# Kernel optimization log

Hardware: AMD Instinct MI355X
Metric: run time of the kernel (lower is better)

Reference implementation:

```python
import jax, jax.numpy as jnp
import numpy as np

B, S, H = 16, 4096, 1024

def setup_inputs() -> dict:
    key = jax.random.key(0)
    k = jax.random.split(key, 6)
    return {
        "query": jax.random.normal(k[0], (B, 1, H), dtype=jnp.float32),
        "proj_key": jax.random.normal(k[1], (B, S, H), dtype=jnp.float32),
        "value": jax.random.normal(k[2], (B, S, 2 * H), dtype=jnp.float32),
        "Wq": jax.random.normal(k[3], (H, H), dtype=jnp.float32) * (1.0 / np.sqrt(H)),
        "we": jax.random.normal(k[4], (H,), dtype=jnp.float32) * (1.0 / np.sqrt(H)),
        "mask": jax.random.randint(k[5], (B, S), 0, 2, dtype=jnp.int32),
    }

def reference(query, proj_key, value, Wq, we, mask):
    # query: [B,1,H]; torch Linear(no bias): y = x @ W^T
    q = jnp.einsum('bqh,oh->bqo', query, Wq)            # [B,1,H]
    e = jnp.tanh(q + proj_key)                          # [B,S,H] (broadcast over S)
    scores = jnp.einsum('bsh,h->bs', e, we)             # energy_layer -> [B,S]
    scores = jnp.where(mask == 0, -jnp.inf, scores)
    alphas = jax.nn.softmax(scores, axis=-1)            # [B,S]
    context = jnp.einsum('bs,bsd->bd', alphas, value)   # bmm([B,1,S],[B,S,2H])
    return context[:, None, :], alphas[:, None, :]
```

## Files before the change

### kernel.cpp

```cpp
#include <hip/hip_runtime.h>
#include <math.h>

#define BATCH 16
#define SEQ   4096
#define HDIM  1024
#define DV    2048
#define NCH   32
#define SCH   (SEQ / NCH)
#define KFT   512

typedef float vf4 __attribute__((ext_vector_type(4)));

__device__ __forceinline__ float tanh_fast(float x) {
    float e = __expf(2.0f * x);
    return 1.0f - 2.0f * __builtin_amdgcn_rcpf(1.0f + e);
}

__device__ __forceinline__ float4 ntload4(const float4* p) {
    vf4 v = __builtin_nontemporal_load((const vf4*)p);
    return make_float4(v.x, v.y, v.z, v.w);
}

__global__ __launch_bounds__(256) void k1_q(const float* __restrict__ query,
                                            const float* __restrict__ Wq,
                                            float* __restrict__ qout) {
    int wave = threadIdx.x >> 6;
    int lane = threadIdx.x & 63;
    int o = blockIdx.x * 4 + wave;
    const float4* wq4 = (const float4*)(Wq + (size_t)o * HDIM);
    float4 w[4];
#pragma unroll
    for (int k = 0; k < 4; ++k) w[k] = wq4[k * 64 + lane];
#pragma unroll
    for (int b = 0; b < BATCH; ++b) {
        const float4* q4 = (const float4*)(query + b * HDIM);
        float acc = 0.f;
#pragma unroll
        for (int k = 0; k < 4; ++k) {
            float4 q = q4[k * 64 + lane];
            acc += w[k].x * q.x + w[k].y * q.y + w[k].z * q.z + w[k].w * q.w;
        }
#pragma unroll
        for (int off = 32; off; off >>= 1) acc += __shfl_down(acc, off, 64);
        if (lane == 0) qout[b * HDIM + o] = acc;
    }
}

__global__ __launch_bounds__(KFT) void kf_fused(const float* __restrict__ pk,
                                                const float* __restrict__ qv,
                                                const float* __restrict__ we,
                                                const int* __restrict__ mask,
                                                const float* __restrict__ value,
                                                float* __restrict__ scores,
                                                float* __restrict__ partial,
                                                float* __restrict__ chunkm,
                                                float* __restrict__ chunkz) {
    int bid = blockIdx.x;
    int b = bid >> 5;
    int c = bid & (NCH - 1);
    int s0 = c * SCH;
    int t = threadIdx.x;
    int wave = t >> 6;
    int lane = t & 63;

    __shared__ float s_sc[SCH];
    __shared__ float s_a[SCH];
    __shared__ int   s_list[SCH];
    __shared__ float s_aa[SCH];
    __shared__ int   s_off[SCH];
    __shared__ int   s_nact;
    __shared__ float redm[8];
    __shared__ float redz[8];

    if (t < 64) {
        int r0 = b * SEQ + s0 + t;
        int p0 = (mask[r0] != 0);
        unsigned long long b0 = __ballot(p0);
        int n0 = __popcll(b0);
        if (p0) {
            s_list[__popcll(b0 & ((1ull << lane) - 1ull))] = t;
        } else {
            s_sc[t] = -INFINITY;
            scores[r0] = -INFINITY;
        }
        int r1 = b * SEQ + s0 + 64 + t;
        int p1 = (mask[r1] != 0);
        unsigned long long b1 = __ballot(p1);
        if (p1) {
            s_list[n0 + __popcll(b1 & ((1ull << lane) - 1ull))] = 64 + t;
        } else {
            s_sc[64 + t] = -INFINITY;
            scores[r1] = -INFINITY;
        }
        if (lane == 0) s_nact = n0 + __popcll(b1);
    }

    const float4* q4  = (const float4*)(qv + b * HDIM);
    const float4* we4 = (const float4*)we;
    float4 qr[4], wr[4];
#pragma unroll
    for (int k = 0; k < 4; ++k) {
        qr[k] = q4[k * 64 + lane];
        wr[k] = we4[k * 64 + lane];
    }
    __syncthreads();
    int nact = s_nact;

    for (int j = wave; j < nact; j += 8) {
        int s = s_list[j];
        int r = b * SEQ + s0 + s;
        const float4* row = (const float4*)(pk + (size_t)r * HDIM);
        float acc = 0.f;
#pragma unroll
        for (int k = 0; k < 4; ++k) {
            float4 p = ntload4(row + k * 64 + lane);
            acc += tanh_fast(p.x + qr[k].x) * wr[k].x;
            acc += tanh_fast(p.y + qr[k].y) * wr[k].y;
            acc += tanh_fast(p.z + qr[k].z) * wr[k].z;
            acc += tanh_fast(p.w + qr[k].w) * wr[k].w;
        }
#pragma unroll
        for (int off = 32; off; off >>= 1) acc += __shfl_down(acc, off, 64);
        if (lane == 0) {
            s_sc[s] = acc;
            scores[r] = acc;
        }
    }
    __syncthreads();

    float mval = (t < SCH) ? s_sc[t] : -INFINITY;
    float mr = mval;
#pragma unroll
    for (int off = 32; off; off >>= 1) mr = fmaxf(mr, __shfl_down(mr, off, 64));
    if (lane == 0) redm[wave] = mr;
    __syncthreads();
    float mc = -INFINITY;
#pragma unroll
    for (int i = 0; i < 8; ++i) mc = fmaxf(mc, redm[i]);

    float av = 0.f;
    if (t < SCH) {
        av = (mval == -INFINITY || mc == -INFINITY) ? 0.f : __expf(mval - mc);
        s_a[t] = av;
    }
    float zr = av;
#pragma unroll
    for (int off = 32; off; off >>= 1) zr += __shfl_down(zr, off, 64);
    if (lane == 0) redz[wave] = zr;
    __syncthreads();
    if (t == 0) {
        float z = 0.f;
#pragma unroll
        for (int i = 0; i < 8; ++i) z += redz[i];
        chunkm[bid] = mc;
        chunkz[bid] = z;
    }
    if (t < SCH && t < nact) {
        int s = s_list[t];
        s_aa[t]  = s_a[s];
        s_off[t] = (s0 + s) * (DV / 4);
    }
    __syncthreads();

    const float4* v4 = (const float4*)(value + (size_t)b * SEQ * DV);
    float4 acc0 = make_float4(0.f, 0.f, 0.f, 0.f);
    float4 acc1 = make_float4(0.f, 0.f, 0.f, 0.f);
    float4 acc2 = make_float4(0.f, 0.f, 0.f, 0.f);
    float4 acc3 = make_float4(0.f, 0.f, 0.f, 0.f);
    int j = 0;
    for (; j + 3 < nact; j += 4) {
        int   o0 = s_off[j],     o1 = s_off[j + 1];
        int   o2 = s_off[j + 2], o3 = s_off[j + 3];
        float w0 = s_aa[j],      w1 = s_aa[j + 1];
        float w2 = s_aa[j + 2],  w3 = s_aa[j + 3];
        float4 u0 = ntload4(v4 + o0 + t);
        float4 u1 = ntload4(v4 + o1 + t);
        float4 u2 = ntload4(v4 + o2 + t);
        float4 u3 = ntload4(v4 + o3 + t);
        acc0.x += w0 * u0.x; acc0.y += w0 * u0.y; acc0.z += w0 * u0.z; acc0.w += w0 * u0.w;
        acc1.x += w1 * u1.x; acc1.y += w1 * u1.y; acc1.z += w1 * u1.z; acc1.w += w1 * u1.w;
        acc2.x += w2 * u2.x; acc2.y += w2 * u2.y; acc2.z += w2 * u2.z; acc2.w += w2 * u2.w;
        acc3.x += w3 * u3.x; acc3.y += w3 * u3.y; acc3.z += w3 * u3.z; acc3.w += w3 * u3.w;
    }
    for (; j < nact; ++j) {
        int   o = s_off[j];
        float w = s_aa[j];
        float4 u = ntload4(v4 + o + t);
        acc0.x += w * u.x; acc0.y += w * u.y; acc0.z += w * u.z; acc0.w += w * u.w;
    }
    acc0.x += acc1.x + acc2.x + acc3.x;
    acc0.y += acc1.y + acc2.y + acc3.y;
    acc0.z += acc1.z + acc2.z + acc3.z;
    acc0.w += acc1.w + acc2.w + acc3.w;
    ((float4*)(partial + (size_t)bid * DV))[t] = acc0;
}

__global__ __launch_bounds__(256) void kz_final(const float* __restrict__ scores,
                                                const float* __restrict__ partial,
                                                const float* __restrict__ chunkm,
                                                const float* __restrict__ chunkz,
                                                float* __restrict__ ctx,
                                                float* __restrict__ alphas) {
    int bid = blockIdx.x;
    int b = bid >> 4;
    int q = bid & 15;
    int t = threadIdx.x;

    __shared__ float s_m[NCH];
    __shared__ float s_z[NCH];
    __shared__ float s_half[128];

    if (t < NCH) {
        s_m[t] = chunkm[b * NCH + t];
        s_z[t] = chunkz[b * NCH + t];
    }
    __syncthreads();

    float m = -INFINITY;
#pragma unroll
    for (int i = 0; i < NCH; ++i) m = fmaxf(m, s_m[i]);
    float Z = 0.f;
#pragma unroll
    for (int i = 0; i < NCH; ++i) {
        float mi = s_m[i];
        if (mi != -INFINITY) Z += s_z[i] * __expf(mi - m);
    }
    float inv = 1.0f / Z;

    {
        float sc = scores[(size_t)b * SEQ + q * 256 + t];
        float e = (sc == -INFINITY) ? 0.f : __expf(sc - m);
        alphas[(size_t)b * SEQ + q * 256 + t] = e * inv;
    }

    int col = q * 128 + (t & 127);
    int half = t >> 7;
    float sum = 0.f;
    const float* pbase = partial + (size_t)b * NCH * DV + col;
#pragma unroll 4
    for (int cc = half * 16; cc < half * 16 + 16; ++cc) {
        float mi = s_m[cc];
        if (mi != -INFINITY) {
            float g = __expf(mi - m);
            sum += g * pbase[(size_t)cc * DV];
        }
    }
    if (half == 1) s_half[t & 127] = sum;
    __syncthreads();
    if (half == 0)
        ctx[(size_t)b * DV + col] = (sum + s_half[t]) * inv;
}

__global__ __launch_bounds__(256) void k2_scores(const float* __restrict__ pk,
                                                 const float* __restrict__ qv,
                                                 const float* __restrict__ we,
                                                 const int* __restrict__ mask,
                                                 float* __restrict__ scores) {
    int wave = threadIdx.x >> 6;
    int lane = threadIdx.x & 63;
    int r = blockIdx.x * 4 + wave;
    int b = r >> 12;
    if (mask[r] == 0) { if (lane == 0) scores[r] = -INFINITY; return; }
    const float4* row = (const float4*)(pk + (size_t)r * HDIM);
    const float4* q4  = (const float4*)(qv + b * HDIM);
    const float4* we4 = (const float4*)we;
    float acc = 0.f;
#pragma unroll
    for (int k = 0; k < 4; ++k) {
        int idx = k * 64 + lane;
        float4 p = row[idx];
        float4 q = q4[idx];
        float4 w = we4[idx];
        acc += tanh_fast(p.x + q.x) * w.x;
        acc += tanh_fast(p.y + q.y) * w.y;
        acc += tanh_fast(p.z + q.z) * w.z;
        acc += tanh_fast(p.w + q.w) * w.w;
    }
#pragma unroll
    for (int off = 32; off; off >>= 1) acc += __shfl_down(acc, off, 64);
    if (lane == 0) scores[r] = acc;
}

__global__ __launch_bounds__(256) void k3_softmax(const float* __restrict__ scores,
                                                  float* __restrict__ alphas) {
    int b = blockIdx.x;
    int t = threadIdx.x;
    const float* sc = scores + b * SEQ;
    float loc[16];
    float m = -INFINITY;
#pragma unroll
    for (int i = 0; i < 16; ++i) { loc[i] = sc[t + i * 256]; m = fmaxf(m, loc[i]); }
#pragma unroll
    for (int off = 32; off; off >>= 1) m = fmaxf(m, __shfl_down(m, off, 64));
    __shared__ float redm[4];
    if ((t & 63) == 0) redm[t >> 6] = m;
    __syncthreads();
    m = fmaxf(fmaxf(redm[0], redm[1]), fmaxf(redm[2], redm[3]));
    float sum = 0.f;
#pragma unroll
    for (int i = 0; i < 16; ++i) {
        loc[i] = (loc[i] == -INFINITY) ? 0.f : __expf(loc[i] - m);
        sum += loc[i];
    }
#pragma unroll
    for (int off = 32; off; off >>= 1) sum += __shfl_down(sum, off, 64);
    __shared__ float reds[4];
    if ((t & 63) == 0) reds[t >> 6] = sum;
    __syncthreads();
    float inv = 1.0f / (reds[0] + reds[1] + reds[2] + reds[3]);
#pragma unroll
    for (int i = 0; i < 16; ++i) alphas[b * SEQ + t + i * 256] = loc[i] * inv;
}

__global__ __launch_bounds__(256) void k4_atomic(const float* __restrict__ value,
                                                 const float* __restrict__ alphas,
                                                 float* __restrict__ ctx) {
    int bid = blockIdx.x;
    int ch = bid & 31;
    int dt = (bid >> 5) & 1;
    int b  = bid >> 6;
    int t  = threadIdx.x;
    const float4* v4 = (const float4*)(value + (size_t)b * SEQ * DV + dt * 1024);
    const float* al = alphas + b * SEQ + ch * 128;
    float4 acc = make_float4(0.f, 0.f, 0.f, 0.f);
    for (int s = 0; s < 128; ++s) {
        float a = al[s];
        if (a != 0.f) {
            float4 v = v4[(size_t)(ch * 128 + s) * (DV / 4) + t];
            acc.x += a * v.x; acc.y += a * v.y; acc.z += a * v.z; acc.w += a * v.w;
        }
    }
    float* dst = ctx + (size_t)b * DV + dt * 1024 + t * 4;
    atomicAdd(dst + 0, acc.x);
    atomicAdd(dst + 1, acc.y);
    atomicAdd(dst + 2, acc.z);
    atomicAdd(dst + 3, acc.w);
}

extern "C" void kernel_launch(void* const* d_in, const int* in_sizes, int n_in,
                              void* d_out, int out_size, void* d_ws, size_t ws_size,
                              hipStream_t stream) {
    const float* query = (const float*)d_in[0];
    const float* pk    = (const float*)d_in[1];
    const float* value = (const float*)d_in[2];
    const float* Wq    = (const float*)d_in[3];
    const float* we    = (const float*)d_in[4];
    const int*   mask  = (const int*)d_in[5];

    float* out    = (float*)d_out;
    float* ctx    = out;
    float* alphas = out + BATCH * DV;

    float* ws      = (float*)d_ws;
    float* qws     = ws;
    float* scores  = ws + BATCH * HDIM;
    float* chunkm  = scores + BATCH * SEQ;
    float* chunkz  = chunkm + BATCH * NCH;
    float* partial = chunkz + BATCH * NCH;

    k1_q<<<HDIM / 4, 256, 0, stream>>>(query, Wq, qws);

    size_t need = (size_t)(BATCH * HDIM + BATCH * SEQ + 2 * BATCH * NCH
                           + (size_t)BATCH * NCH * DV) * sizeof(float);
    if (ws_size >= need) {
        kf_fused<<<BATCH * NCH, KFT, 0, stream>>>(pk, qws, we, mask, value,
                                                  scores, partial, chunkm, chunkz);
        kz_final<<<BATCH * 16, 256, 0, stream>>>(scores, partial, chunkm, chunkz,
                                                 ctx, alphas);
    } else {
        k2_scores<<<(BATCH * SEQ) / 4, 256, 0, stream>>>(pk, qws, we, mask, scores);
        k3_softmax<<<BATCH, 256, 0, stream>>>(scores, alphas);
        (void)hipMemsetAsync(ctx, 0, (size_t)BATCH * DV * sizeof(float), stream);
        k4_atomic<<<BATCH * 64, 256, 0, stream>>>(value, alphas, ctx);
    }
}
```

Measured before the change: 90.78 us.

## Compact active rows per batch and split them evenly across chunks

Adds a per-batch compaction kernel that prefix-scans the mask into a global list of active row indices and a per-batch count. Each fused block now takes an equal share of the active rows instead of a fixed span of sequence positions, so the work per block no longer depends on how the mask happens to fall. This costs one extra small kernel launch and a round trip through global memory for the row list, and the fused kernel's per-chunk softmax statistics now cover arbitrary subsets of rows.

Result: no change. 92.34 us (+1.7%).

```diff
diff --git a/kernel.cpp b/kernel.cpp
--- a/kernel.cpp
+++ b/kernel.cpp
@@ -46,11 +46,53 @@
     }
 }
 
+__global__ __launch_bounds__(1024) void kc_compact(const int* __restrict__ mask,
+                                                   int* __restrict__ rowlist,
+                                                   int* __restrict__ nacts,
+                                                   float* __restrict__ scores) {
+    int b = blockIdx.x;
+    int t = threadIdx.x;
+    int wave = t >> 6, lane = t & 63;
+    __shared__ int wtot[16];
+    __shared__ int wbase[16];
+
+    int4 mv = ((const int4*)(mask + (size_t)b * SEQ))[t];
+    int m0 = (mv.x != 0), m1 = (mv.y != 0), m2 = (mv.z != 0), m3 = (mv.w != 0);
+    int cnt = m0 + m1 + m2 + m3;
+
+    int scan = cnt;
+#pragma unroll
+    for (int off = 1; off < 64; off <<= 1) {
+        int n = __shfl_up(scan, off, 64);
+        if (lane >= off) scan += n;
+    }
+    int excl = scan - cnt;
+    if (lane == 63) wtot[wave] = scan;
+    __syncthreads();
+    if (t == 0) {
+        int run = 0;
+#pragma unroll
+        for (int i = 0; i < 16; ++i) { wbase[i] = run; run += wtot[i]; }
+        nacts[b] = run;
+    }
+    __syncthreads();
+
+    int base = wbase[wave] + excl;
+    int* dst = rowlist + (size_t)b * SEQ;
+    float* scb = scores + (size_t)b * SEQ;
+    int r = 4 * t;
+    if (m0) dst[base++] = r;     else scb[r]     = -INFINITY;
+    if (m1) dst[base++] = r + 1; else scb[r + 1] = -INFINITY;
+    if (m2) dst[base++] = r + 2; else scb[r + 2] = -INFINITY;
+    if (m3) dst[base++] = r + 3; else scb[r + 3] = -INFINITY;
+}
+
 __global__ __launch_bounds__(KFT) void kf_fused(const float* __restrict__ pk,
                                                 const float* __restrict__ qv,
                                                 const float* __restrict__ we,
-                                                const int* __restrict__ mask,
                                                 const float* __restrict__ value,
+                                                const int* __restrict__ rowlist,
+                                                const int* __restrict__ nacts,
                                                 float* __restrict__ scores,
                                                 float* __restrict__ partial,
                                                 float* __restrict__ chunkm,
@@ -58,42 +100,25 @@
     int bid = blockIdx.x;
     int b = bid >> 5;
     int c = bid & (NCH - 1);
-    int s0 = c * SCH;
     int t = threadIdx.x;
     int wave = t >> 6;
     int lane = t & 63;
 
     __shared__ float s_sc[SCH];
-    __shared__ float s_a[SCH];
     __shared__ int   s_list[SCH];
     __shared__ float s_aa[SCH];
     __shared__ int   s_off[SCH];
-    __shared__ int   s_nact;
     __shared__ float redm[8];
     __shared__ float redz[8];
 
-    if (t < 64) {
-        int r0 = b * SEQ + s0 + t;
-        int p0 = (mask[r0] != 0);
-        unsigned long long b0 = __ballot(p0);
-        int n0 = __popcll(b0);
-        if (p0) {
-            s_list[__popcll(b0 & ((1ull << lane) - 1ull))] = t;
-        } else {
-            s_sc[t] = -INFINITY;
-            scores[r0] = -INFINITY;
-        }
-        int r1 = b * SEQ + s0 + 64 + t;
-        int p1 = (mask[r1] != 0);
-        unsigned long long b1 = __ballot(p1);
-        if (p1) {
-            s_list[n0 + __popcll(b1 & ((1ull << lane) - 1ull))] = 64 + t;
-        } else {
-            s_sc[64 + t] = -INFINITY;
-            scores[r1] = -INFINITY;
-        }
-        if (lane == 0) s_nact = n0 + __popcll(b1);
-    }
+    int nact_b = nacts[b];
+    int len = (nact_b + NCH - 1) >> 5;
+    int j0 = c * len;
+    int cnt = nact_b - j0;
+    if (cnt > len) cnt = len;
+    if (cnt < 0) cnt = 0;
+
+    if (t < cnt) s_list[t] = rowlist[(size_t)b * SEQ + j0 + t];
 
     const float4* q4  = (const float4*)(qv + b * HDIM);
     const float4* we4 = (const float4*)we;
@@ -104,12 +129,10 @@
         wr[k] = we4[k * 64 + lane];
     }
     __syncthreads();
-    int nact = s_nact;
-
-    for (int j = wave; j < nact; j += 8) {
+
+    for (int j = wave; j < cnt; j += 8) {
         int s = s_list[j];
-        int r = b * SEQ + s0 + s;
-        const float4* row = (const float4*)(pk + (size_t)r * HDIM);
+        const float4* row = (const float4*)(pk + ((size_t)b * SEQ + s) * HDIM);
         float acc = 0.f;
 #pragma unroll
         for (int k = 0; k < 4; ++k) {
@@ -122,13 +145,13 @@
 #pragma unroll
         for (int off = 32; off; off >>= 1) acc += __shfl_down(acc, off, 64);
         if (lane == 0) {
-            s_sc[s] = acc;
-            scores[r] = acc;
+            s_sc[j] = acc;
+            scores[(size_t)b * SEQ + s] = acc;
         }
     }
     __syncthreads();
 
-    float mval = (t < SCH) ? s_sc[t] : -INFINITY;
+    float mval = (t < cnt) ? s_sc[t] : -INFINITY;
     float mr = mval;
 #pragma unroll
     for (int off = 32; off; off >>= 1) mr = fmaxf(mr, __shfl_down(mr, off, 64));
@@ -139,9 +162,10 @@
     for (int i = 0; i < 8; ++i) mc = fmaxf(mc, redm[i]);
 
     float av = 0.f;
-    if (t < SCH) {
-        av = (mval == -INFINITY || mc == -INFINITY) ? 0.f : __expf(mval - mc);
-        s_a[t] = av;
+    if (t < cnt) {
+        av = __expf(mval - mc);
+        s_aa[t]  = av;
+        s_off[t] = s_list[t] * (DV / 4);
     }
     float zr = av;
 #pragma unroll
@@ -154,11 +178,6 @@
         for (int i = 0; i < 8; ++i) z += redz[i];
         chunkm[bid] = mc;
         chunkz[bid] = z;
-    }
-    if (t < SCH && t < nact) {
-        int s = s_list[t];
-        s_aa[t]  = s_a[s];
-        s_off[t] = (s0 + s) * (DV / 4);
     }
     __syncthreads();
 
@@ -168,7 +187,7 @@
     float4 acc2 = make_float4(0.f, 0.f, 0.f, 0.f);
     float4 acc3 = make_float4(0.f, 0.f, 0.f, 0.f);
     int j = 0;
-    for (; j + 3 < nact; j += 4) {
+    for (; j + 3 < cnt; j += 4) {
         int   o0 = s_off[j],     o1 = s_off[j + 1];
         int   o2 = s_off[j + 2], o3 = s_off[j + 3];
         float w0 = s_aa[j],      w1 = s_aa[j + 1];
@@ -182,7 +201,7 @@
         acc2.x += w2 * u2.x; acc2.y += w2 * u2.y; acc2.z += w2 * u2.z; acc2.w += w2 * u2.w;
         acc3.x += w3 * u3.x; acc3.y += w3 * u3.y; acc3.z += w3 * u3.z; acc3.w += w3 * u3.w;
     }
-    for (; j < nact; ++j) {
+    for (; j < cnt; ++j) {
         int   o = s_off[j];
         float w = s_aa[j];
         float4 u = ntload4(v4 + o + t);
@@ -357,13 +376,18 @@
     float* chunkm  = scores + BATCH * SEQ;
     float* chunkz  = chunkm + BATCH * NCH;
     float* partial = chunkz + BATCH * NCH;
+    int*   rowlist = (int*)(partial + (size_t)BATCH * NCH * DV);
+    int*   nacts   = rowlist + BATCH * SEQ;
+
+    size_t need = ((size_t)(BATCH * HDIM + BATCH * SEQ + 2 * BATCH * NCH
+                            + (size_t)BATCH * NCH * DV) +
+                   (size_t)(BATCH * SEQ + BATCH)) * sizeof(float);
 
     k1_q<<<HDIM / 4, 256, 0, stream>>>(query, Wq, qws);
 
-    size_t need = (size_t)(BATCH * HDIM + BATCH * SEQ + 2 * BATCH * NCH
-                           + (size_t)BATCH * NCH * DV) * sizeof(float);
     if (ws_size >= need) {
-        kf_fused<<<BATCH * NCH, KFT, 0, stream>>>(pk, qws, we, mask, value,
+        kc_compact<<<BATCH, 1024, 0, stream>>>(mask, rowlist, nacts, scores);
+        kf_fused<<<BATCH * NCH, KFT, 0, stream>>>(pk, qws, we, value, rowlist, nacts,
                                                   scores, partial, chunkm, chunkz);
         kz_final<<<BATCH * 16, 256, 0, stream>>>(scores, partial, chunkm, chunkz,
                                                  ctx, alphas);
```
